# Optimization experiments

Hardware: AMD Instinct MI355X
Metric: run time of the kernel (lower is better)

## Reference

```python
import jax, jax.numpy as jnp
import numpy as np

M, N, T = 4, 48, 512
D_IN = M + N                 # GRU-net input dim (m+n)
H1 = D_IN * 10 * 8           # 4160
HID = M * M + N * N          # 2320 GRU hidden
H2 = M * N * 4               # 768
D_OUT = M * N                # 192


def setup_inputs() -> dict:
    key = jax.random.key(0)
    ks = jax.random.split(key, 12)
    s = lambda i, shape, sc=0.02: (jax.random.normal(ks[i], shape, jnp.float32) * sc)
    return {
        "A": jnp.eye(M, dtype=jnp.float32) + s(0, (M, M), 0.05),
        "C": s(1, (N, M + 1), 0.1),
        "x0": jax.random.normal(ks[2], (M,), jnp.float32),
        "h0": jax.random.normal(ks[3], (HID,), jnp.float32),  # randn init hidden (zero_hidden_state=False)
        "y_seq": jax.random.normal(ks[4], (N, T), jnp.float32),
        "W1": s(5, (H1, D_IN)), "b1": jnp.zeros((H1,), jnp.float32),
        "W_ih": s(6, (3 * HID, H1)), "W_hh": s(7, (3 * HID, HID)),
        "b_ih": jnp.zeros((3 * HID,), jnp.float32), "b_hh": jnp.zeros((3 * HID,), jnp.float32),
        "W2": s(8, (H2, HID)), "b2": jnp.zeros((H2,), jnp.float32),
        "W3": s(9, (D_OUT, H2)), "b3": jnp.zeros((D_OUT,), jnp.float32),
    }


def _l2norm(v):
    # torch F.normalize(p=2, eps=1e-12): v / max(||v||, eps)
    return v / jnp.maximum(jnp.linalg.norm(v), 1e-12)


def _gru_cell(x, h, W_ih, W_hh, b_ih, b_hh):
    gi = W_ih @ x + b_ih
    gh = W_hh @ h + b_hh
    i_r, i_z, i_n = jnp.split(gi, 3)
    h_r, h_z, h_n = jnp.split(gh, 3)
    r = jax.nn.sigmoid(i_r + h_r)
    z = jax.nn.sigmoid(i_z + h_z)
    n = jnp.tanh(i_n + r * h_n)
    return (1.0 - z) * n + z * h


def reference(A, C, x0, h0, y_seq, W1, b1, W_ih, W_hh, b_ih, b_hh, W2, b2, W3, b3):
    one = jnp.ones((1,), jnp.float32)

    def step(carry, y):
        x_prior, x_post, h = carry
        # step_prior (linear case)
        x_prev_prior = x_prior
        x_prior = A @ x_post
        m1y = C @ jnp.concatenate([x_prior, one])  # [N]
        # step_KGain_est: KGainNet_in = [norm(dy), norm(dx)]
        knet_in = jnp.concatenate([_l2norm(y - m1y), _l2norm(x_post - x_prev_prior)])
        l1 = jax.nn.relu(W1 @ knet_in + b1)
        h = _gru_cell(l1, h, W_ih, W_hh, b_ih, b_hh)
        l2 = jax.nn.relu(W2 @ h + b2)
        kg = ((W3 @ l2 + b3) / 10000.0).reshape(M, N)
        # KNet_step posterior update
        x_post = x_prior + kg @ (y - m1y)
        return (x_prior, x_post, h), x_post

    _, xs = jax.lax.scan(step, (x0, x0, h0), y_seq.T)  # scan over T
    return xs.T  # [M, T], matches forward_sequence output
```

## Files before the change

kernel.cpp:

```cpp
#include <hip/hip_runtime.h>
#include <stdint.h>
#include <stddef.h>

typedef float v2f __attribute__((ext_vector_type(2)));

#define HID   2320
#define G3    6960
#define KIH   4160
#define KHH   2320
#define NBLK  232
#define NL2B  192
#define NTHR  512
#define UPB   10
#define TSEQ  512
#define KRES  1600
#define INVWS (1.0f/128.0f)
#define SPINCAP (1u<<17)

#define WS_WIH8 0L
#define WS_W1E  28953600L
#define WS_HBP  29219840L
#define WS_SLT  29279232L
#define WS_END  29308928L

struct Offs {
  int l1s, hs, wih, whh, w2s, w3s, cs, as_, b3s, bih, bhh, b2s, gis, ghs,
      ts, inn, kn, dxs, xpri, xpo, b4, nrm, l2r, slp;
  int total;
};

__host__ __device__ inline Offs mkoffs(int res) {
  Offs o; int p = 0;
#define ALLOC(name, bytes) { p = (p + 15) & ~15; o.name = p; p += (bytes); }
  ALLOC(l1s, KIH*4) ALLOC(hs, HID*4)
  ALLOC(wih, res ? 30*KRES : 16) ALLOC(whh, res ? 30*KHH : 16)
  ALLOC(w2s, res ? 4*HID : 16)
  ALLOC(w3s, 16*48*4) ALLOC(cs, 240*4) ALLOC(as_, 64) ALLOC(b3s, 192*4)
  ALLOC(bih, 120) ALLOC(bhh, 120) ALLOC(b2s, 16)
  ALLOC(gis, 120) ALLOC(ghs, 120)
  ALLOC(ts, 64) ALLOC(inn, 192) ALLOC(kn, 256)
  ALLOC(dxs, 16) ALLOC(xpri, 16) ALLOC(xpo, 16) ALLOC(b4, 16) ALLOC(nrm, 16)
  ALLOC(l2r, 16) ALLOC(slp, 64)
#undef ALLOC
  o.total = (p + 63) & ~63;
  return o;
}

struct Params {
  const float *A, *C, *x0, *h0, *y, *W1, *b1, *Wih, *Whh, *bih, *bhh, *W2, *b2, *W3, *b3;
  const uint8_t *wih8, *w1e;
  uint64_t *hbp, *slt;
  float *out;
  int resident;
};

__device__ __forceinline__ uint8_t f2fp8(float v) {
  v = fminf(fmaxf(v * 128.f, -448.f), 448.f);
  int pk = __builtin_amdgcn_cvt_pk_fp8_f32(v, v, 0, false);
  return (uint8_t)(pk & 0xff);
}

__device__ __forceinline__ void pub64(uint64_t* a, uint32_t tag, float v) {
  uint64_t w = ((uint64_t)tag << 32) | (uint64_t)__float_as_uint(v);
  __hip_atomic_store(a, w, __ATOMIC_RELAXED, __HIP_MEMORY_SCOPE_AGENT);
}

template<int N>
__device__ __forceinline__ void poll_pkt(const uint64_t* base, uint32_t want,
                                         float* out, bool& dead) {
  uint64_t v[N];
  uint32_t spins = 0;
  for (;;) {
    bool ok = true;
#pragma unroll
    for (int k = 0; k < N; ++k)
      v[k] = __hip_atomic_load(base + k, __ATOMIC_RELAXED, __HIP_MEMORY_SCOPE_AGENT);
#pragma unroll
    for (int k = 0; k < N; ++k) ok &= ((uint32_t)(v[k] >> 32) == want);
    if (ok || dead) break;
    ++spins;
    if (spins > 8) __builtin_amdgcn_s_sleep(2);
    if (spins > SPINCAP) dead = true;
  }
#pragma unroll
  for (int k = 0; k < N; ++k) out[k] = __uint_as_float((uint32_t)v[k]);
}

__device__ __forceinline__ void dot8_lds(
    const float* __restrict__ acts, const uint8_t* __restrict__ w, int stride,
    int K, const int* lrows, int nr, int lane, float acc[4])
{
  int kb = 0;
  for (; kb + 256 <= K; kb += 256) {
    const float4 a = ((const float4*)(acts + kb))[lane];
#pragma unroll
    for (int j = 0; j < 4; ++j) if (j < nr) {
      uint32_t wb = *(const uint32_t*)(w + (size_t)lrows[j]*stride + kb + (lane<<2));
      v2f lo = __builtin_amdgcn_cvt_pk_f32_fp8((int)wb, false);
      v2f hi = __builtin_amdgcn_cvt_pk_f32_fp8((int)wb, true);
      acc[j] = fmaf(lo.x, a.x, acc[j]); acc[j] = fmaf(lo.y, a.y, acc[j]);
      acc[j] = fmaf(hi.x, a.z, acc[j]); acc[j] = fmaf(hi.y, a.w, acc[j]);
    }
  }
  int rem = K - kb;
  if ((lane << 2) < rem) {
    const float4 a = ((const float4*)(acts + kb))[lane];
#pragma unroll
    for (int j = 0; j < 4; ++j) if (j < nr) {
      uint32_t wb = *(const uint32_t*)(w + (size_t)lrows[j]*stride + kb + (lane<<2));
      v2f lo = __builtin_amdgcn_cvt_pk_f32_fp8((int)wb, false);
      v2f hi = __builtin_amdgcn_cvt_pk_f32_fp8((int)wb, true);
      acc[j] = fmaf(lo.x, a.x, acc[j]); acc[j] = fmaf(lo.y, a.y, acc[j]);
      acc[j] = fmaf(hi.x, a.z, acc[j]); acc[j] = fmaf(hi.y, a.w, acc[j]);
    }
  }
}

__device__ __forceinline__ void dot8_glb(
    const float* __restrict__ acts, const uint8_t* __restrict__ gw, int gstride,
    int K0, int K, const int* grows, int nr, int lane, float acc[4])
{
  int kb = K0;
  for (; kb + 512 <= K; kb += 512) {
    const float4 a0 = ((const float4*)(acts + kb))[lane*2];
    const float4 a1 = ((const float4*)(acts + kb))[lane*2 + 1];
#pragma unroll
    for (int j = 0; j < 4; ++j) if (j < nr) {
      uint2 wb = *(const uint2*)(gw + (size_t)grows[j]*gstride + kb + (lane<<3));
      v2f l0 = __builtin_amdgcn_cvt_pk_f32_fp8((int)wb.x, false);
      v2f h0 = __builtin_amdgcn_cvt_pk_f32_fp8((int)wb.x, true);
      v2f l1 = __builtin_amdgcn_cvt_pk_f32_fp8((int)wb.y, false);
      v2f h1 = __builtin_amdgcn_cvt_pk_f32_fp8((int)wb.y, true);
      acc[j] = fmaf(l0.x, a0.x, acc[j]); acc[j] = fmaf(l0.y, a0.y, acc[j]);
      acc[j] = fmaf(h0.x, a0.z, acc[j]); acc[j] = fmaf(h0.y, a0.w, acc[j]);
      acc[j] = fmaf(l1.x, a1.x, acc[j]); acc[j] = fmaf(l1.y, a1.y, acc[j]);
      acc[j] = fmaf(h1.x, a1.z, acc[j]); acc[j] = fmaf(h1.y, a1.w, acc[j]);
    }
  }
  for (int e = kb + lane; e < K; e += 64) {
    float a = acts[e];
#pragma unroll
    for (int j = 0; j < 4; ++j) if (j < nr) {
      v2f lo = __builtin_amdgcn_cvt_pk_f32_fp8(
          (int)(uint32_t)gw[(size_t)grows[j]*gstride + e], false);
      acc[j] = fmaf(lo.x, a, acc[j]);
    }
  }
}

__device__ __forceinline__ void dotf_glb(
    const float* __restrict__ acts, const float* __restrict__ gw, int gstride,
    int K, const int* grows, int nr, int lane, float acc[4])
{
  for (int k = lane; k < K; k += 64) {
    float a = acts[k];
#pragma unroll
    for (int j = 0; j < 4; ++j) if (j < nr)
      acc[j] = fmaf(gw[(size_t)grows[j]*gstride + k], a, acc[j]);
  }
}

extern "C" __global__ void __launch_bounds__(NTHR, 2) knet_main(Params p)
{
  extern __shared__ char smem[];
  const Offs o = mkoffs(p.resident);
  float*   L1S  = (float*)(smem + o.l1s);
  float*   HS   = (float*)(smem + o.hs);
  uint8_t* WIHR = (uint8_t*)(smem + o.wih);
  uint8_t* WHHR = (uint8_t*)(smem + o.whh);
  uint8_t* W2S  = (uint8_t*)(smem + o.w2s);
  float*   W3S  = (float*)(smem + o.w3s);
  float*   CS   = (float*)(smem + o.cs);
  float*   AS   = (float*)(smem + o.as_);
  float*   B3S  = (float*)(smem + o.b3s);
  float*   BIH  = (float*)(smem + o.bih);
  float*   BHH  = (float*)(smem + o.bhh);
  float*   B2S  = (float*)(smem + o.b2s);
  float*   GIS  = (float*)(smem + o.gis);
  float*   GHS  = (float*)(smem + o.ghs);
  float*   TS   = (float*)(smem + o.ts);
  float*   INNS = (float*)(smem + o.inn);
  float*   KN   = (float*)(smem + o.kn);
  float*   DXS  = (float*)(smem + o.dxs);
  float*   XPRI = (float*)(smem + o.xpri);
  float*   XPO  = (float*)(smem + o.xpo);
  float*   B4   = (float*)(smem + o.b4);
  float*   NRM  = (float*)(smem + o.nrm);
  float*   L2R  = (float*)(smem + o.l2r);
  float*   SLP  = (float*)(smem + o.slp);

  const int tid  = (int)threadIdx.x;
  const int bid  = (int)blockIdx.x;
  const int lane = tid & 63;
  const int wv   = tid >> 6;
  const int rows2 = (bid < NL2B) ? 4 : 0;
  const int r2s   = bid * 4;
  bool dead = false;

  int lrows[4] = {0,0,0,0}, grows[4] = {0,0,0,0};
  int nr = 0;
#pragma unroll
  for (int j = 0; j < 4; ++j) {
    int row = wv + 8*j;
    if (row < 30) { int u = row/3, g = row - 3*u;
      lrows[nr] = row; grows[nr] = g*HID + bid*UPB + u; ++nr; }
  }

  for (int i = tid; i < rows2*192; i += NTHR) { int rl = i/192, rem = i - rl*192;
    W3S[i] = p.W3[(size_t)rem*768 + (r2s + rl)]; }
  for (int i = tid; i < 240; i += NTHR) CS[i] = p.C[i];
  if (tid < 16) AS[tid] = p.A[tid];
  for (int i = tid; i < 192; i += NTHR) B3S[i] = p.b3[i];
  if (tid < rows2) B2S[tid] = p.b2[r2s + tid];
  if (tid < 30) {
    int u = tid/3, g = tid - 3*u, ug = bid*UPB + u;
    BIH[tid] = p.bih[g*HID + ug];
    BHH[tid] = p.bhh[g*HID + ug];
  }
  for (int i = tid; i < HID; i += NTHR) HS[i] = p.h0[i];
  if (p.resident) {
    const int kd = KRES >> 2;
    uint32_t* W32 = (uint32_t*)WIHR;
    for (int i = tid; i < 30*kd; i += NTHR) {
      int row = i / kd, c = i - row*kd;
      int u = row/3, g = row - 3*u, gr = g*HID + bid*UPB + u;
      W32[i] = ((const uint32_t*)p.wih8)[(size_t)gr*(KIH/4) + c];
    }
    for (int i = tid; i < 30*KHH; i += NTHR) {
      int row = i / KHH, k = i - row*KHH;
      int u = row/3, g = row - 3*u, gr = g*HID + bid*UPB + u;
      WHHR[i] = f2fp8(p.Whh[(size_t)gr*KHH + k]);
    }
    for (int i = tid; i < rows2*HID; i += NTHR) {
      int rl = i / HID, k = i - rl*HID;
      W2S[i] = f2fp8(p.W2[(size_t)(r2s+rl)*HID + k]);
    }
  }
  uint2 pf[4][5];
#pragma unroll
  for (int j = 0; j < 4; ++j)
#pragma unroll
    for (int i = 0; i < 5; ++i) pf[j][i] = make_uint2(0u, 0u);
#pragma unroll
  for (int j = 0; j < 4; ++j) if (j < nr)
#pragma unroll
    for (int i = 0; i < 5; ++i)
      pf[j][i] = *(const uint2*)(p.wih8 + (size_t)grows[j]*KIH + KRES + i*512 + (lane<<3));
  __syncthreads();

  auto small_chain = [&](int ycol) {
    if (tid < 48) {
      float s = CS[tid*5 + 4];
#pragma unroll
      for (int k = 0; k < 4; ++k) s += CS[tid*5 + k] * XPRI[k];
      INNS[tid] = p.y[(size_t)tid*TSEQ + ycol] - s;
    }
    __syncthreads();
    if (wv == 0) {
      float q = (lane < 48) ? INNS[lane]*INNS[lane] : 0.f;
#pragma unroll
      for (int m = 32; m >= 1; m >>= 1) q += __shfl_xor(q, m, 64);
      if (lane == 0) NRM[0] = fmaxf(sqrtf(q), 1e-12f);
    } else if (wv == 1) {
      float q = (lane < 4) ? DXS[lane]*DXS[lane] : 0.f;
#pragma unroll
      for (int m = 32; m >= 1; m >>= 1) q += __shfl_xor(q, m, 64);
      if (lane == 0) NRM[1] = fmaxf(sqrtf(q), 1e-12f);
    }
    __syncthreads();
    if (tid < 48) KN[tid] = INNS[tid] / NRM[0];
    else if (tid < 52) KN[tid] = DXS[tid-48] / NRM[1];
    else if (tid == 52) KN[tid] = 1.0f;
    else if (tid < 64) KN[tid] = 0.0f;
    else if (tid < 68) {
      int i = tid - 64; float s = 0;
      for (int j = 0; j < 48; ++j) s += B3S[i*48 + j] * INNS[j];
      B4[i] = s;
    }
    if (tid >= 128 && tid < 128 + rows2*4) {
      int idx = tid - 128, rl = idx >> 2, i = idx & 3;
      float s = 0;
      for (int j = 0; j < 48; ++j) s += W3S[rl*192 + i*48 + j] * INNS[j];
      TS[i*4 + rl] = s;
    }
    __syncthreads();
    {
      float4 kn[16];
#pragma unroll
      for (int c = 0; c < 16; ++c) kn[c] = ((const float4*)KN)[c];
      for (int r = tid; r < KIH; r += NTHR) {
        const uint4* wp = (const uint4*)(p.w1e + (size_t)r*64);
        float acc = 0.f;
#pragma unroll
        for (int q = 0; q < 4; ++q) {
          uint4 w = wp[q];
          v2f l0 = __builtin_amdgcn_cvt_pk_f32_fp8((int)w.x, false);
          v2f h0 = __builtin_amdgcn_cvt_pk_f32_fp8((int)w.x, true);
          v2f l1 = __builtin_amdgcn_cvt_pk_f32_fp8((int)w.y, false);
          v2f h1 = __builtin_amdgcn_cvt_pk_f32_fp8((int)w.y, true);
          v2f l2 = __builtin_amdgcn_cvt_pk_f32_fp8((int)w.z, false);
          v2f h2 = __builtin_amdgcn_cvt_pk_f32_fp8((int)w.z, true);
          v2f l3 = __builtin_amdgcn_cvt_pk_f32_fp8((int)w.w, false);
          v2f h3 = __builtin_amdgcn_cvt_pk_f32_fp8((int)w.w, true);
          float4 a0 = kn[q*4+0], a1 = kn[q*4+1], a2 = kn[q*4+2], a3 = kn[q*4+3];
          acc = fmaf(l0.x,a0.x,acc); acc = fmaf(l0.y,a0.y,acc);
          acc = fmaf(h0.x,a0.z,acc); acc = fmaf(h0.y,a0.w,acc);
          acc = fmaf(l1.x,a1.x,acc); acc = fmaf(l1.y,a1.y,acc);
          acc = fmaf(h1.x,a1.z,acc); acc = fmaf(h1.y,a1.w,acc);
          acc = fmaf(l2.x,a2.x,acc); acc = fmaf(l2.y,a2.y,acc);
          acc = fmaf(h2.x,a2.z,acc); acc = fmaf(h2.y,a2.w,acc);
          acc = fmaf(l3.x,a3.x,acc); acc = fmaf(l3.y,a3.y,acc);
          acc = fmaf(h3.x,a3.z,acc); acc = fmaf(h3.y,a3.w,acc);
        }
        L1S[r] = fmaxf(acc * INVWS, 0.f);
      }
    }
    __syncthreads();
  };

  auto ghh = [&]() {
    float acc[4] = {0,0,0,0};
    if (p.resident) dot8_lds(HS, WHHR, KHH, KHH, lrows, nr, lane, acc);
    else            dotf_glb(HS, p.Whh, KHH, KHH, grows, nr, lane, acc);
#pragma unroll
    for (int m = 32; m >= 1; m >>= 1)
#pragma unroll
      for (int j = 0; j < 4; ++j) acc[j] += __shfl_xor(acc[j], m, 64);
    if (lane == 0)
#pragma unroll
      for (int j = 0; j < 4; ++j) if (j < nr) GHS[lrows[j]] = acc[j];
  };

  if (tid < 4) { XPO[tid] = p.x0[tid]; DXS[tid] = 0.f; }
  __syncthreads();
  if (tid < 4) {
    float s = 0;
#pragma unroll
    for (int j = 0; j < 4; ++j) s += AS[tid*4 + j] * XPO[j];
    XPRI[tid] = s;
  }
  __syncthreads();
  small_chain(0);
  ghh();
  __syncthreads();

  for (int t = 0; t < TSEQ; ++t) {
    const int par = t & 1;
    const uint32_t want = (uint32_t)(t + 1);

    {
      float acc[4] = {0,0,0,0};
      if (p.resident) dot8_lds(L1S, WIHR, KRES, KRES, lrows, nr, lane, acc);
      else            dot8_glb(L1S, p.wih8, KIH, 0, KRES, grows, nr, lane, acc);
#pragma unroll
      for (int i = 0; i < 5; ++i) {
        const float4 a0 = ((const float4*)(L1S + KRES + i*512))[lane*2];
        const float4 a1 = ((const float4*)(L1S + KRES + i*512))[lane*2 + 1];
#pragma unroll
        for (int j = 0; j < 4; ++j) if (j < nr) {
          uint2 w = pf[j][i];
          v2f l0 = __builtin_amdgcn_cvt_pk_f32_fp8((int)w.x, false);
          v2f h0 = __builtin_amdgcn_cvt_pk_f32_fp8((int)w.x, true);
          v2f l1v = __builtin_amdgcn_cvt_pk_f32_fp8((int)w.y, false);
          v2f h1 = __builtin_amdgcn_cvt_pk_f32_fp8((int)w.y, true);
          acc[j] = fmaf(l0.x, a0.x, acc[j]); acc[j] = fmaf(l0.y, a0.y, acc[j]);
          acc[j] = fmaf(h0.x, a0.z, acc[j]); acc[j] = fmaf(h0.y, a0.w, acc[j]);
          acc[j] = fmaf(l1v.x, a1.x, acc[j]); acc[j] = fmaf(l1v.y, a1.y, acc[j]);
          acc[j] = fmaf(h1.x, a1.z, acc[j]); acc[j] = fmaf(h1.y, a1.w, acc[j]);
        }
      }
#pragma unroll
      for (int m = 32; m >= 1; m >>= 1)
#pragma unroll
        for (int j = 0; j < 4; ++j) acc[j] += __shfl_xor(acc[j], m, 64);
      if (lane == 0)
#pragma unroll
        for (int j = 0; j < 4; ++j) if (j < nr) GIS[lrows[j]] = acc[j];
    }
    __syncthreads();

    if (tid < UPB) {
      int ug = bid*UPB + tid, r0 = tid*3;
      float gi0 = GIS[r0+0]*INVWS + BIH[r0+0], gh0 = GHS[r0+0]*INVWS + BHH[r0+0];
      float gi1 = GIS[r0+1]*INVWS + BIH[r0+1], gh1 = GHS[r0+1]*INVWS + BHH[r0+1];
      float gi2 = GIS[r0+2]*INVWS + BIH[r0+2], gh2 = GHS[r0+2]*INVWS + BHH[r0+2];
      float rg = 1.f/(1.f + expf(-(gi0+gh0)));
      float zg = 1.f/(1.f + expf(-(gi1+gh1)));
      float ng = tanhf(gi2 + rg*gh2);
      float hnew = (1.f - zg)*ng + zg*HS[ug];
      pub64(p.hbp + (((size_t)par*NBLK + bid) << 4) + tid, want, hnew);
    }
    __syncthreads();

    if (wv < 4) {
      int idx = (wv << 6) | lane;
      if (idx < NBLK) {
        float v[10];
        poll_pkt<10>(p.hbp + (((size_t)par*NBLK + idx) << 4), want, v, dead);
#pragma unroll
        for (int k = 0; k < 10; ++k) HS[idx*10 + k] = v[k];
      }
    }
    __syncthreads();

    if (rows2 && wv >= 4) {
      const int rl = wv - 4;
      float a2 = 0.f;
      if (p.resident) {
        int kb = 0;
        for (; kb + 256 <= HID; kb += 256) {
          const float4 a = ((const float4*)(HS + kb))[lane];
          uint32_t wb = *(const uint32_t*)(W2S + rl*HID + kb + (lane<<2));
          v2f lo = __builtin_amdgcn_cvt_pk_f32_fp8((int)wb, false);
          v2f hi = __builtin_amdgcn_cvt_pk_f32_fp8((int)wb, true);
          a2 = fmaf(lo.x, a.x, a2); a2 = fmaf(lo.y, a.y, a2);
          a2 = fmaf(hi.x, a.z, a2); a2 = fmaf(hi.y, a.w, a2);
        }
        if ((lane << 2) < HID - kb) {
          const float4 a = ((const float4*)(HS + kb))[lane];
          uint32_t wb = *(const uint32_t*)(W2S + rl*HID + kb + (lane<<2));
          v2f lo = __builtin_amdgcn_cvt_pk_f32_fp8((int)wb, false);
          v2f hi = __builtin_amdgcn_cvt_pk_f32_fp8((int)wb, true);
          a2 = fmaf(lo.x, a.x, a2); a2 = fmaf(lo.y, a.y, a2);
          a2 = fmaf(hi.x, a.z, a2); a2 = fmaf(hi.y, a.w, a2);
        }
        a2 *= INVWS;
      } else {
        for (int k = lane; k < HID; k += 64)
          a2 = fmaf(p.W2[(size_t)(r2s+rl)*HID + k], HS[k], a2);
      }
#pragma unroll
      for (int m = 32; m >= 1; m >>= 1) a2 += __shfl_xor(a2, m, 64);
      if (lane == 0) L2R[rl] = fmaxf(a2 + B2S[rl], 0.f);
    }
    __syncthreads();
    if (rows2 && tid < 4) {
      float cp = L2R[0]*TS[tid*4+0] + L2R[1]*TS[tid*4+1]
               + L2R[2]*TS[tid*4+2] + L2R[3]*TS[tid*4+3];
      pub64(p.slt + (((size_t)par*NBLK + bid) << 3) + tid, want, cp);
    }

    ghh();

    if (wv < 3) {
      int idx = (wv << 6) | lane;
      float v[4];
      poll_pkt<4>(p.slt + (((size_t)par*NBLK + idx) << 3), want, v, dead);
      float s0 = v[0], s1 = v[1], s2 = v[2], s3 = v[3];
#pragma unroll
      for (int m = 32; m >= 1; m >>= 1) {
        s0 += __shfl_xor(s0, m, 64); s1 += __shfl_xor(s1, m, 64);
        s2 += __shfl_xor(s2, m, 64); s3 += __shfl_xor(s3, m, 64);
      }
      if (lane == 0) {
        SLP[wv*4+0] = s0; SLP[wv*4+1] = s1; SLP[wv*4+2] = s2; SLP[wv*4+3] = s3;
      }
    }
    __syncthreads();

    if (tid < 4) {
      float c = SLP[tid] + SLP[4 + tid] + SLP[8 + tid];
      float xp = XPRI[tid] + (c + B4[tid]) * 1e-4f;
      XPO[tid] = xp;
      if (bid == 0) p.out[(size_t)tid*TSEQ + t] = xp;
    }
    __syncthreads();
    if (t + 1 < TSEQ) {
      if (tid < 4) {
        float xo = XPO[tid];
        DXS[tid] = xo - XPRI[tid];
        float s = 0;
#pragma unroll
        for (int j = 0; j < 4; ++j) s += AS[tid*4 + j] * XPO[j];
        XPRI[tid] = s;
      }
      __syncthreads();
      small_chain(t + 1);
    }
  }
}

extern "C" __global__ void knet_cvt_fp8(const float* __restrict__ src,
                                        uint8_t* __restrict__ dst, long n4) {
  long stride = (long)gridDim.x * blockDim.x;
  for (long i = (long)blockIdx.x*blockDim.x + threadIdx.x; i < n4; i += stride) {
    float4 v = ((const float4*)src)[i];
    float a0 = fminf(fmaxf(v.x * 128.f, -448.f), 448.f);
    float a1 = fminf(fmaxf(v.y * 128.f, -448.f), 448.f);
    float a2 = fminf(fmaxf(v.z * 128.f, -448.f), 448.f);
    float a3 = fminf(fmaxf(v.w * 128.f, -448.f), 448.f);
    int pk = __builtin_amdgcn_cvt_pk_fp8_f32(a0, a1, 0, false);
    pk = __builtin_amdgcn_cvt_pk_fp8_f32(a2, a3, pk, true);
    ((uint32_t*)dst)[i] = (uint32_t)pk;
  }
}

extern "C" __global__ void knet_build_w1e(const float* __restrict__ W1,
                                          const float* __restrict__ b1,
                                          uint8_t* __restrict__ dst) {
  int r = blockIdx.x * blockDim.x + threadIdx.x;
  if (r >= KIH) return;
  float v[64];
#pragma unroll 13
  for (int q = 0; q < 13; ++q) {
    float4 w = ((const float4*)(W1 + (size_t)r*52))[q];
    v[q*4+0] = w.x; v[q*4+1] = w.y; v[q*4+2] = w.z; v[q*4+3] = w.w;
  }
  v[52] = b1[r];
  for (int i = 53; i < 64; ++i) v[i] = 0.f;
  uint32_t out[16];
#pragma unroll 16
  for (int d = 0; d < 16; ++d) {
    float a0 = fminf(fmaxf(v[d*4+0] * 128.f, -448.f), 448.f);
    float a1 = fminf(fmaxf(v[d*4+1] * 128.f, -448.f), 448.f);
    float a2 = fminf(fmaxf(v[d*4+2] * 128.f, -448.f), 448.f);
    float a3 = fminf(fmaxf(v[d*4+3] * 128.f, -448.f), 448.f);
    int pk = __builtin_amdgcn_cvt_pk_fp8_f32(a0, a1, 0, false);
    pk = __builtin_amdgcn_cvt_pk_fp8_f32(a2, a3, pk, true);
    out[d] = (uint32_t)pk;
  }
  uint4* dp = (uint4*)(dst + (size_t)r*64);
#pragma unroll 4
  for (int q = 0; q < 4; ++q)
    dp[q] = make_uint4(out[q*4+0], out[q*4+1], out[q*4+2], out[q*4+3]);
}

extern "C" void kernel_launch(void* const* d_in, const int* in_sizes, int n_in,
                              void* d_out, int out_size, void* d_ws, size_t ws_size,
                              hipStream_t stream)
{
  if (ws_size < (size_t)WS_END) return;
  uint8_t* ws = (uint8_t*)d_ws;

  knet_cvt_fp8<<<2048, 256, 0, stream>>>((const float*)d_in[7], ws + WS_WIH8,
                                         (long)G3*KIH/4);
  knet_build_w1e<<<(KIH + 255)/256, 256, 0, stream>>>(
      (const float*)d_in[5], (const float*)d_in[6], ws + WS_W1E);

  int resident = 1;
  Offs o = mkoffs(resident);
  hipError_t e = hipFuncSetAttribute((const void*)knet_main,
                                     hipFuncAttributeMaxDynamicSharedMemorySize,
                                     o.total);
  if (e != hipSuccess) {
    resident = 0; o = mkoffs(resident);
    (void)hipFuncSetAttribute((const void*)knet_main,
                              hipFuncAttributeMaxDynamicSharedMemorySize, o.total);
  }

  Params p;
  p.A   = (const float*)d_in[0];  p.C   = (const float*)d_in[1];
  p.x0  = (const float*)d_in[2];  p.h0  = (const float*)d_in[3];
  p.y   = (const float*)d_in[4];
  p.W1  = (const float*)d_in[5];  p.b1  = (const float*)d_in[6];
  p.Wih = (const float*)d_in[7];  p.Whh = (const float*)d_in[8];
  p.bih = (const float*)d_in[9];  p.bhh = (const float*)d_in[10];
  p.W2  = (const float*)d_in[11]; p.b2  = (const float*)d_in[12];
  p.W3  = (const float*)d_in[13]; p.b3  = (const float*)d_in[14];
  p.wih8 = ws + WS_WIH8;
  p.w1e  = ws + WS_W1E;
  p.hbp  = (uint64_t*)(ws + WS_HBP);
  p.slt  = (uint64_t*)(ws + WS_SLT);
  p.out  = (float*)d_out;
  p.resident = resident;

  knet_main<<<NBLK, NTHR, (size_t)o.total, stream>>>(p);
}
```

Before: 8.289 ms.

## Keep W1 rows in registers, poll single flag first, drop GRU barrier

Each thread now preloads the first four 512-row chunks of the fp8 W1 matrix into registers once, so the per-step layer-1 matvec reads those rows from registers instead of global memory. The GRU hidden element owned by each thread is kept in a register (myh), which removes the read of HS and allows the barrier between publishing h and polling peers to be dropped. Polling now spins on the first packet word alone before checking the rest, which cuts the number of atomic loads per spin iteration. The cost is higher register pressure, about 64 extra VGPRs for the W1 cache, which may lower occupancy or cause spills.

```diff
diff --git a/kernel.cpp b/kernel.cpp
--- a/kernel.cpp
+++ b/kernel.cpp
@@ -14,6 +14,7 @@
 #define UPB   10
 #define TSEQ  512
 #define KRES  1600
+#define HQ    4
 #define INVWS (1.0f/128.0f)
 #define SPINCAP (1u<<17)
 
@@ -68,22 +69,55 @@
 template<int N>
 __device__ __forceinline__ void poll_pkt(const uint64_t* base, uint32_t want,
                                          float* out, bool& dead) {
-  uint64_t v[N];
+  uint64_t v0;
   uint32_t spins = 0;
   for (;;) {
-    bool ok = true;
-#pragma unroll
-    for (int k = 0; k < N; ++k)
-      v[k] = __hip_atomic_load(base + k, __ATOMIC_RELAXED, __HIP_MEMORY_SCOPE_AGENT);
-#pragma unroll
-    for (int k = 0; k < N; ++k) ok &= ((uint32_t)(v[k] >> 32) == want);
-    if (ok || dead) break;
+    v0 = __hip_atomic_load(base, __ATOMIC_RELAXED, __HIP_MEMORY_SCOPE_AGENT);
+    if ((uint32_t)(v0 >> 32) == want || dead) break;
     ++spins;
-    if (spins > 8) __builtin_amdgcn_s_sleep(2);
+    if (spins > 32) __builtin_amdgcn_s_sleep(2);
     if (spins > SPINCAP) dead = true;
   }
-#pragma unroll
-  for (int k = 0; k < N; ++k) out[k] = __uint_as_float((uint32_t)v[k]);
+  out[0] = __uint_as_float((uint32_t)v0);
+  if (N > 1) {
+    uint64_t v[N];
+    uint32_t s2 = 0;
+    for (;;) {
+      bool ok = true;
+#pragma unroll
+      for (int k = 1; k < N; ++k)
+        v[k] = __hip_atomic_load(base + k, __ATOMIC_RELAXED, __HIP_MEMORY_SCOPE_AGENT);
+#pragma unroll
+      for (int k = 1; k < N; ++k) ok &= ((uint32_t)(v[k] >> 32) == want);
+      if (ok || dead) break;
+      ++s2;
+      if (s2 > 8) __builtin_amdgcn_s_sleep(2);
+      if (s2 > SPINCAP) dead = true;
+    }
+#pragma unroll
+    for (int k = 1; k < N; ++k) out[k] = __uint_as_float((uint32_t)v[k]);
+  }
+}
+
+__device__ __forceinline__ float fma16(uint4 w, float4 a0, float4 a1,
+                                       float4 a2, float4 a3, float acc) {
+  v2f l0 = __builtin_amdgcn_cvt_pk_f32_fp8((int)w.x, false);
+  v2f h0 = __builtin_amdgcn_cvt_pk_f32_fp8((int)w.x, true);
+  v2f l1 = __builtin_amdgcn_cvt_pk_f32_fp8((int)w.y, false);
+  v2f h1 = __builtin_amdgcn_cvt_pk_f32_fp8((int)w.y, true);
+  v2f l2 = __builtin_amdgcn_cvt_pk_f32_fp8((int)w.z, false);
+  v2f h2 = __builtin_amdgcn_cvt_pk_f32_fp8((int)w.z, true);
+  v2f l3 = __builtin_amdgcn_cvt_pk_f32_fp8((int)w.w, false);
+  v2f h3 = __builtin_amdgcn_cvt_pk_f32_fp8((int)w.w, true);
+  acc = fmaf(l0.x,a0.x,acc); acc = fmaf(l0.y,a0.y,acc);
+  acc = fmaf(h0.x,a0.z,acc); acc = fmaf(h0.y,a0.w,acc);
+  acc = fmaf(l1.x,a1.x,acc); acc = fmaf(l1.y,a1.y,acc);
+  acc = fmaf(h1.x,a1.z,acc); acc = fmaf(h1.y,a1.w,acc);
+  acc = fmaf(l2.x,a2.x,acc); acc = fmaf(l2.y,a2.y,acc);
+  acc = fmaf(h2.x,a2.z,acc); acc = fmaf(h2.y,a2.w,acc);
+  acc = fmaf(l3.x,a3.x,acc); acc = fmaf(l3.y,a3.y,acc);
+  acc = fmaf(h3.x,a3.z,acc); acc = fmaf(h3.y,a3.w,acc);
+  return acc;
 }
 
 __device__ __forceinline__ void dot8_lds(
@@ -218,6 +252,7 @@
     BHH[tid] = p.bhh[g*HID + ug];
   }
   for (int i = tid; i < HID; i += NTHR) HS[i] = p.h0[i];
+  float myh = (tid < UPB) ? p.h0[(size_t)bid*UPB + tid] : 0.f;
   if (p.resident) {
     const int kd = KRES >> 2;
     uint32_t* W32 = (uint32_t*)WIHR;
@@ -246,6 +281,13 @@
 #pragma unroll
     for (int i = 0; i < 5; ++i)
       pf[j][i] = *(const uint2*)(p.wih8 + (size_t)grows[j]*KIH + KRES + i*512 + (lane<<3));
+  uint4 w1h[HQ][4];
+#pragma unroll
+  for (int h = 0; h < HQ; ++h) {
+    const uint4* wp = (const uint4*)(p.w1e + (size_t)(tid + h*NTHR)*64);
+#pragma unroll
+    for (int q = 0; q < 4; ++q) w1h[h][q] = wp[q];
+  }
   __syncthreads();
 
   auto small_chain = [&](int ycol) {
@@ -288,29 +330,21 @@
       float4 kn[16];
 #pragma unroll
       for (int c = 0; c < 16; ++c) kn[c] = ((const float4*)KN)[c];
-      for (int r = tid; r < KIH; r += NTHR) {
+#pragma unroll
+      for (int h = 0; h < HQ; ++h) {
+        float acc = 0.f;
+#pragma unroll
+        for (int q = 0; q < 4; ++q)
+          acc = fma16(w1h[h][q], kn[q*4+0], kn[q*4+1], kn[q*4+2], kn[q*4+3], acc);
+        L1S[tid + h*NTHR] = fmaxf(acc * INVWS, 0.f);
+      }
+      for (int r = tid + HQ*NTHR; r < KIH; r += NTHR) {
         const uint4* wp = (const uint4*)(p.w1e + (size_t)r*64);
         float acc = 0.f;
 #pragma unroll
         for (int q = 0; q < 4; ++q) {
           uint4 w = wp[q];
-          v2f l0 = __builtin_amdgcn_cvt_pk_f32_fp8((int)w.x, false);
-          v2f h0 = __builtin_amdgcn_cvt_pk_f32_fp8((int)w.x, true);
-          v2f l1 = __builtin_amdgcn_cvt_pk_f32_fp8((int)w.y, false);
-          v2f h1 = __builtin_amdgcn_cvt_pk_f32_fp8((int)w.y, true);
-          v2f l2 = __builtin_amdgcn_cvt_pk_f32_fp8((int)w.z, false);
-          v2f h2 = __builtin_amdgcn_cvt_pk_f32_fp8((int)w.z, true);
-          v2f l3 = __builtin_amdgcn_cvt_pk_f32_fp8((int)w.w, false);
-          v2f h3 = __builtin_amdgcn_cvt_pk_f32_fp8((int)w.w, true);
-          float4 a0 = kn[q*4+0], a1 = kn[q*4+1], a2 = kn[q*4+2], a3 = kn[q*4+3];
-          acc = fmaf(l0.x,a0.x,acc); acc = fmaf(l0.y,a0.y,acc);
-          acc = fmaf(h0.x,a0.z,acc); acc = fmaf(h0.y,a0.w,acc);
-          acc = fmaf(l1.x,a1.x,acc); acc = fmaf(l1.y,a1.y,acc);
-          acc = fmaf(h1.x,a1.z,acc); acc = fmaf(h1.y,a1.w,acc);
-          acc = fmaf(l2.x,a2.x,acc); acc = fmaf(l2.y,a2.y,acc);
-          acc = fmaf(h2.x,a2.z,acc); acc = fmaf(h2.y,a2.w,acc);
-          acc = fmaf(l3.x,a3.x,acc); acc = fmaf(l3.y,a3.y,acc);
-          acc = fmaf(h3.x,a3.z,acc); acc = fmaf(h3.y,a3.w,acc);
+          acc = fma16(w, kn[q*4+0], kn[q*4+1], kn[q*4+2], kn[q*4+3], acc);
         }
         L1S[r] = fmaxf(acc * INVWS, 0.f);
       }
@@ -380,17 +414,17 @@
     __syncthreads();
 
     if (tid < UPB) {
-      int ug = bid*UPB + tid, r0 = tid*3;
+      int r0 = tid*3;
       float gi0 = GIS[r0+0]*INVWS + BIH[r0+0], gh0 = GHS[r0+0]*INVWS + BHH[r0+0];
       float gi1 = GIS[r0+1]*INVWS + BIH[r0+1], gh1 = GHS[r0+1]*INVWS + BHH[r0+1];
       float gi2 = GIS[r0+2]*INVWS + BIH[r0+2], gh2 = GHS[r0+2]*INVWS + BHH[r0+2];
       float rg = 1.f/(1.f + expf(-(gi0+gh0)));
       float zg = 1.f/(1.f + expf(-(gi1+gh1)));
       float ng = tanhf(gi2 + rg*gh2);
-      float hnew = (1.f - zg)*ng + zg*HS[ug];
+      float hnew = (1.f - zg)*ng + zg*myh;
+      myh = hnew;
       pub64(p.hbp + (((size_t)par*NBLK + bid) << 4) + tid, want, hnew);
     }
-    __syncthreads();
 
     if (wv < 4) {
       int idx = (wv << 6) | lane;
```

Measured after the change: 28.31 ms. 3.41x slower.

## Precompute next-step W1 innovation product early and overlap it with GRU stages

Applied to the files above, without the earlier changes.

The innovation for step t+1 is split algebraically into a part that depends only on the prior state, y_{t+1} - C·A·x_prior, and a correction that is linear in dx. The W1 product for that first part is computed in chunks on idle waves during the hidden-state gather, layer-2 and ghh phases, so the serial per-step layer-1 matvec shrinks to a cheap finish pass. The finish pass applies the dx correction through precomputed W1·C·A columns stored as fp16 in spare w1e slots, then normalises, adds the bias and applies ReLU. The own-unit hidden value is kept in a register, which lets one barrier be dropped. The cost is added numerical approximation from the fp16/fp8 correction terms and more complex scheduling across waves.

```diff
diff --git a/kernel.cpp b/kernel.cpp
--- a/kernel.cpp
+++ b/kernel.cpp
@@ -1,4 +1,5 @@
 #include <hip/hip_runtime.h>
+#include <hip/hip_fp16.h>
 #include <stdint.h>
 #include <stddef.h>
 
@@ -14,6 +15,8 @@
 #define UPB   10
 #define TSEQ  512
 #define KRES  1600
+#define CH0   2080
+#define CH1   2336
 #define INVWS (1.0f/128.0f)
 #define SPINCAP (1u<<17)
 
@@ -25,7 +28,7 @@
 
 struct Offs {
   int l1s, hs, wih, whh, w2s, w3s, cs, as_, b3s, bih, bhh, b2s, gis, ghs,
-      ts, inn, kn, dxs, xpri, xpo, b4, nrm, l2r, slp;
+      ts, inn, inn0, xq, cma, dxs, xpri, xpo, b4, nrm, l2r, slp;
   int total;
 };
 
@@ -38,7 +41,7 @@
   ALLOC(w3s, 16*48*4) ALLOC(cs, 240*4) ALLOC(as_, 64) ALLOC(b3s, 192*4)
   ALLOC(bih, 120) ALLOC(bhh, 120) ALLOC(b2s, 16)
   ALLOC(gis, 120) ALLOC(ghs, 120)
-  ALLOC(ts, 64) ALLOC(inn, 192) ALLOC(kn, 256)
+  ALLOC(ts, 64) ALLOC(inn, 192) ALLOC(inn0, 192) ALLOC(xq, 16) ALLOC(cma, 768)
   ALLOC(dxs, 16) ALLOC(xpri, 16) ALLOC(xpo, 16) ALLOC(b4, 16) ALLOC(nrm, 16)
   ALLOC(l2r, 16) ALLOC(slp, 64)
 #undef ALLOC
@@ -84,6 +87,27 @@
   }
 #pragma unroll
   for (int k = 0; k < N; ++k) out[k] = __uint_as_float((uint32_t)v[k]);
+}
+
+__device__ __forceinline__ float fma16(uint4 w, float4 a0, float4 a1,
+                                       float4 a2, float4 a3, float acc) {
+  v2f l0 = __builtin_amdgcn_cvt_pk_f32_fp8((int)w.x, false);
+  v2f h0 = __builtin_amdgcn_cvt_pk_f32_fp8((int)w.x, true);
+  v2f l1 = __builtin_amdgcn_cvt_pk_f32_fp8((int)w.y, false);
+  v2f h1 = __builtin_amdgcn_cvt_pk_f32_fp8((int)w.y, true);
+  v2f l2 = __builtin_amdgcn_cvt_pk_f32_fp8((int)w.z, false);
+  v2f h2 = __builtin_amdgcn_cvt_pk_f32_fp8((int)w.z, true);
+  v2f l3 = __builtin_amdgcn_cvt_pk_f32_fp8((int)w.w, false);
+  v2f h3 = __builtin_amdgcn_cvt_pk_f32_fp8((int)w.w, true);
+  acc = fmaf(l0.x,a0.x,acc); acc = fmaf(l0.y,a0.y,acc);
+  acc = fmaf(h0.x,a0.z,acc); acc = fmaf(h0.y,a0.w,acc);
+  acc = fmaf(l1.x,a1.x,acc); acc = fmaf(l1.y,a1.y,acc);
+  acc = fmaf(h1.x,a1.z,acc); acc = fmaf(h1.y,a1.w,acc);
+  acc = fmaf(l2.x,a2.x,acc); acc = fmaf(l2.y,a2.y,acc);
+  acc = fmaf(h2.x,a2.z,acc); acc = fmaf(h2.y,a2.w,acc);
+  acc = fmaf(l3.x,a3.x,acc); acc = fmaf(l3.y,a3.y,acc);
+  acc = fmaf(h3.x,a3.z,acc); acc = fmaf(h3.y,a3.w,acc);
+  return acc;
 }
 
 __device__ __forceinline__ void dot8_lds(
@@ -180,7 +204,9 @@
   float*   GHS  = (float*)(smem + o.ghs);
   float*   TS   = (float*)(smem + o.ts);
   float*   INNS = (float*)(smem + o.inn);
-  float*   KN   = (float*)(smem + o.kn);
+  float*   INN0 = (float*)(smem + o.inn0);
+  float*   XQ   = (float*)(smem + o.xq);
+  float*   CMA  = (float*)(smem + o.cma);
   float*   DXS  = (float*)(smem + o.dxs);
   float*   XPRI = (float*)(smem + o.xpri);
   float*   XPO  = (float*)(smem + o.xpo);
@@ -218,6 +244,7 @@
     BHH[tid] = p.bhh[g*HID + ug];
   }
   for (int i = tid; i < HID; i += NTHR) HS[i] = p.h0[i];
+  float myh = (tid < UPB) ? p.h0[(size_t)bid*UPB + tid] : 0.f;
   if (p.resident) {
     const int kd = KRES >> 2;
     uint32_t* W32 = (uint32_t*)WIHR;
@@ -248,74 +275,43 @@
       pf[j][i] = *(const uint2*)(p.wih8 + (size_t)grows[j]*KIH + KRES + i*512 + (lane<<3));
   __syncthreads();
 
-  auto small_chain = [&](int ycol) {
-    if (tid < 48) {
-      float s = CS[tid*5 + 4];
-#pragma unroll
-      for (int k = 0; k < 4; ++k) s += CS[tid*5 + k] * XPRI[k];
-      INNS[tid] = p.y[(size_t)tid*TSEQ + ycol] - s;
-    }
-    __syncthreads();
-    if (wv == 0) {
-      float q = (lane < 48) ? INNS[lane]*INNS[lane] : 0.f;
-#pragma unroll
-      for (int m = 32; m >= 1; m >>= 1) q += __shfl_xor(q, m, 64);
-      if (lane == 0) NRM[0] = fmaxf(sqrtf(q), 1e-12f);
-    } else if (wv == 1) {
-      float q = (lane < 4) ? DXS[lane]*DXS[lane] : 0.f;
-#pragma unroll
-      for (int m = 32; m >= 1; m >>= 1) q += __shfl_xor(q, m, 64);
-      if (lane == 0) NRM[1] = fmaxf(sqrtf(q), 1e-12f);
-    }
-    __syncthreads();
-    if (tid < 48) KN[tid] = INNS[tid] / NRM[0];
-    else if (tid < 52) KN[tid] = DXS[tid-48] / NRM[1];
-    else if (tid == 52) KN[tid] = 1.0f;
-    else if (tid < 64) KN[tid] = 0.0f;
-    else if (tid < 68) {
-      int i = tid - 64; float s = 0;
-      for (int j = 0; j < 48; ++j) s += B3S[i*48 + j] * INNS[j];
-      B4[i] = s;
-    }
-    if (tid >= 128 && tid < 128 + rows2*4) {
-      int idx = tid - 128, rl = idx >> 2, i = idx & 3;
-      float s = 0;
-      for (int j = 0; j < 48; ++j) s += W3S[rl*192 + i*48 + j] * INNS[j];
-      TS[i*4 + rl] = s;
-    }
-    __syncthreads();
-    {
-      float4 kn[16];
-#pragma unroll
-      for (int c = 0; c < 16; ++c) kn[c] = ((const float4*)KN)[c];
-      for (int r = tid; r < KIH; r += NTHR) {
-        const uint4* wp = (const uint4*)(p.w1e + (size_t)r*64);
-        float acc = 0.f;
-#pragma unroll
-        for (int q = 0; q < 4; ++q) {
-          uint4 w = wp[q];
-          v2f l0 = __builtin_amdgcn_cvt_pk_f32_fp8((int)w.x, false);
-          v2f h0 = __builtin_amdgcn_cvt_pk_f32_fp8((int)w.x, true);
-          v2f l1 = __builtin_amdgcn_cvt_pk_f32_fp8((int)w.y, false);
-          v2f h1 = __builtin_amdgcn_cvt_pk_f32_fp8((int)w.y, true);
-          v2f l2 = __builtin_amdgcn_cvt_pk_f32_fp8((int)w.z, false);
-          v2f h2 = __builtin_amdgcn_cvt_pk_f32_fp8((int)w.z, true);
-          v2f l3 = __builtin_amdgcn_cvt_pk_f32_fp8((int)w.w, false);
-          v2f h3 = __builtin_amdgcn_cvt_pk_f32_fp8((int)w.w, true);
-          float4 a0 = kn[q*4+0], a1 = kn[q*4+1], a2 = kn[q*4+2], a3 = kn[q*4+3];
-          acc = fmaf(l0.x,a0.x,acc); acc = fmaf(l0.y,a0.y,acc);
-          acc = fmaf(h0.x,a0.z,acc); acc = fmaf(h0.y,a0.w,acc);
-          acc = fmaf(l1.x,a1.x,acc); acc = fmaf(l1.y,a1.y,acc);
-          acc = fmaf(h1.x,a1.z,acc); acc = fmaf(h1.y,a1.w,acc);
-          acc = fmaf(l2.x,a2.x,acc); acc = fmaf(l2.y,a2.y,acc);
-          acc = fmaf(h2.x,a2.z,acc); acc = fmaf(h2.y,a2.w,acc);
-          acc = fmaf(l3.x,a3.x,acc); acc = fmaf(l3.y,a3.y,acc);
-          acc = fmaf(h3.x,a3.z,acc); acc = fmaf(h3.y,a3.w,acc);
-        }
-        L1S[r] = fmaxf(acc * INVWS, 0.f);
-      }
-    }
-    __syncthreads();
+  if (tid < 192) {
+    int j = tid >> 2, k = tid & 3;
+    CMA[tid] = CS[j*5+0]*AS[0*4+k] + CS[j*5+1]*AS[1*4+k]
+             + CS[j*5+2]*AS[2*4+k] + CS[j*5+3]*AS[3*4+k];
+  }
+
+  auto l1a_chunk = [&](int lo, int hi, int tbase, int tcnt) {
+    float4 in0[12];
+#pragma unroll
+    for (int c = 0; c < 12; ++c) in0[c] = ((const float4*)INN0)[c];
+    for (int r = lo + (tid - tbase); r < hi; r += tcnt) {
+      const uint4* wp = (const uint4*)(p.w1e + (size_t)r*64);
+      uint4 w0 = wp[0], w1 = wp[1], w2 = wp[2];
+      float acc = 0.f;
+      acc = fma16(w0, in0[0], in0[1], in0[2],  in0[3],  acc);
+      acc = fma16(w1, in0[4], in0[5], in0[6],  in0[7],  acc);
+      acc = fma16(w2, in0[8], in0[9], in0[10], in0[11], acc);
+      L1S[r] = acc;
+    }
+  };
+
+  auto l1_finish = [&]() {
+    float d0 = DXS[0], d1 = DXS[1], d2 = DXS[2], d3 = DXS[3];
+    float invn0 = 1.f / NRM[0], invn1 = 1.f / NRM[1];
+    float n0 = d0*invn1, n1 = d1*invn1, n2 = d2*invn1, n3 = d3*invn1;
+    for (int r = tid; r < KIH; r += NTHR) {
+      uint4 w = *(const uint4*)(p.w1e + (size_t)r*64 + 48);
+      v2f dq0 = __builtin_amdgcn_cvt_pk_f32_fp8((int)w.x, false);
+      v2f dq1 = __builtin_amdgcn_cvt_pk_f32_fp8((int)w.x, true);
+      v2f bq  = __builtin_amdgcn_cvt_pk_f32_fp8((int)w.y, false);
+      float2 c01 = __half22float2(*(const __half2*)&w.z);
+      float2 c23 = __half22float2(*(const __half2*)&w.w);
+      float corr = c01.x*d0 + c01.y*d1 + c23.x*d2 + c23.y*d3;
+      float acc = (L1S[r] - corr) * invn0
+                + dq0.x*n0 + dq0.y*n1 + dq1.x*n2 + dq1.y*n3 + bq.x;
+      L1S[r] = fmaxf(acc * INVWS, 0.f);
+    }
   };
 
   auto ghh = [&]() {
@@ -340,7 +336,51 @@
     XPRI[tid] = s;
   }
   __syncthreads();
-  small_chain(0);
+  if (tid < 48) {
+    float s = CS[tid*5 + 4];
+#pragma unroll
+    for (int k = 0; k < 4; ++k) s += CS[tid*5 + k] * XPRI[k];
+    float i0 = p.y[(size_t)tid*TSEQ + 0] - s;
+    INN0[tid] = i0; INNS[tid] = i0;
+  } else if (tid >= 64 && tid < 68) {
+    int k = tid - 64; float s = 0;
+#pragma unroll
+    for (int j = 0; j < 4; ++j) s += AS[k*4 + j] * XPRI[j];
+    XQ[k] = s;
+  }
+  __syncthreads();
+  if (wv == 0) {
+    float q = (lane < 48) ? INNS[lane]*INNS[lane] : 0.f;
+#pragma unroll
+    for (int m = 32; m >= 1; m >>= 1) q += __shfl_xor(q, m, 64);
+    if (lane == 0) NRM[0] = fmaxf(sqrtf(q), 1e-12f);
+  } else if (wv == 1) {
+    float q = (lane < 4) ? DXS[lane]*DXS[lane] : 0.f;
+#pragma unroll
+    for (int m = 32; m >= 1; m >>= 1) q += __shfl_xor(q, m, 64);
+    if (lane == 0) NRM[1] = fmaxf(sqrtf(q), 1e-12f);
+  }
+  if (tid >= 128 && tid < 132) {
+    int i = tid - 128; float s = 0;
+    for (int j = 0; j < 48; ++j) s += B3S[i*48 + j] * INNS[j];
+    B4[i] = s;
+  }
+  if (rows2 && tid >= 192 && tid < 208) {
+    int idx = tid - 192, rl = idx >> 2, i = idx & 3;
+    float s = 0;
+    for (int j = 0; j < 48; ++j) s += W3S[rl*192 + i*48 + j] * INNS[j];
+    TS[i*4 + rl] = s;
+  }
+  __syncthreads();
+  l1a_chunk(0, KIH, 0, NTHR);
+  l1_finish();
+  __syncthreads();
+  if (tid < 48) {
+    float s = CS[tid*5 + 4];
+#pragma unroll
+    for (int k = 0; k < 4; ++k) s += CS[tid*5 + k] * XQ[k];
+    INN0[tid] = p.y[(size_t)tid*TSEQ + 1] - s;
+  }
   ghh();
   __syncthreads();
 
@@ -380,17 +420,17 @@
     __syncthreads();
 
     if (tid < UPB) {
-      int ug = bid*UPB + tid, r0 = tid*3;
+      int r0 = tid*3;
       float gi0 = GIS[r0+0]*INVWS + BIH[r0+0], gh0 = GHS[r0+0]*INVWS + BHH[r0+0];
       float gi1 = GIS[r0+1]*INVWS + BIH[r0+1], gh1 = GHS[r0+1]*INVWS + BHH[r0+1];
       float gi2 = GIS[r0+2]*INVWS + BIH[r0+2], gh2 = GHS[r0+2]*INVWS + BHH[r0+2];
       float rg = 1.f/(1.f + expf(-(gi0+gh0)));
       float zg = 1.f/(1.f + expf(-(gi1+gh1)));
       float ng = tanhf(gi2 + rg*gh2);
-      float hnew = (1.f - zg)*ng + zg*HS[ug];
+      float hnew = (1.f - zg)*ng + zg*myh;
+      myh = hnew;
       pub64(p.hbp + (((size_t)par*NBLK + bid) << 4) + tid, want, hnew);
     }
-    __syncthreads();
 
     if (wv < 4) {
       int idx = (wv << 6) | lane;
@@ -400,6 +440,8 @@
 #pragma unroll
         for (int k = 0; k < 10; ++k) HS[idx*10 + k] = v[k];
       }
+    } else if (t + 1 < TSEQ) {
+      l1a_chunk(0, CH0, 256, 256);
     }
     __syncthreads();
 
@@ -432,6 +474,8 @@
 #pragma unroll
       for (int m = 32; m >= 1; m >>= 1) a2 += __shfl_xor(a2, m, 64);
       if (lane == 0) L2R[rl] = fmaxf(a2 + B2S[rl], 0.f);
+    } else if (wv < 4 && t + 1 < TSEQ) {
+      l1a_chunk(CH0, CH1, 0, 256);
     }
     __syncthreads();
     if (rows2 && tid < 4) {
@@ -441,6 +485,7 @@
     }
 
     ghh();
+    if (t + 1 < TSEQ) l1a_chunk(CH1, KIH, 0, NTHR);
 
     if (wv < 3) {
       int idx = (wv << 6) | lane;
@@ -465,6 +510,7 @@
       if (bid == 0) p.out[(size_t)tid*TSEQ + t] = xp;
     }
     __syncthreads();
+
     if (t + 1 < TSEQ) {
       if (tid < 4) {
         float xo = XPO[tid];
@@ -475,7 +521,48 @@
         XPRI[tid] = s;
       }
       __syncthreads();
-      small_chain(t + 1);
+      if (tid < 48) {
+        float dv = CMA[tid*4+0]*DXS[0] + CMA[tid*4+1]*DXS[1]
+                 + CMA[tid*4+2]*DXS[2] + CMA[tid*4+3]*DXS[3];
+        INNS[tid] = INN0[tid] - dv;
+      } else if (tid >= 64 && tid < 68) {
+        int k = tid - 64; float s = 0;
+#pragma unroll
+        for (int j = 0; j < 4; ++j) s += AS[k*4 + j] * XPRI[j];
+        XQ[k] = s;
+      }
+      __syncthreads();
+      if (wv == 0) {
+        float q = (lane < 48) ? INNS[lane]*INNS[lane] : 0.f;
+#pragma unroll
+        for (int m = 32; m >= 1; m >>= 1) q += __shfl_xor(q, m, 64);
+        if (lane == 0) NRM[0] = fmaxf(sqrtf(q), 1e-12f);
+      } else if (wv == 1) {
+        float q = (lane < 4) ? DXS[lane]*DXS[lane] : 0.f;
+#pragma unroll
+        for (int m = 32; m >= 1; m >>= 1) q += __shfl_xor(q, m, 64);
+        if (lane == 0) NRM[1] = fmaxf(sqrtf(q), 1e-12f);
+      }
+      if (tid >= 128 && tid < 132) {
+        int i = tid - 128; float s = 0;
+        for (int j = 0; j < 48; ++j) s += B3S[i*48 + j] * INNS[j];
+        B4[i] = s;
+      }
+      if (rows2 && tid >= 192 && tid < 208) {
+        int idx = tid - 192, rl = idx >> 2, i = idx & 3;
+        float s = 0;
+        for (int j = 0; j < 48; ++j) s += W3S[rl*192 + i*48 + j] * INNS[j];
+        TS[i*4 + rl] = s;
+      }
+      __syncthreads();
+      if (tid < 48 && t + 2 < TSEQ) {
+        float s = CS[tid*5 + 4];
+#pragma unroll
+        for (int k = 0; k < 4; ++k) s += CS[tid*5 + k] * XQ[k];
+        INN0[tid] = p.y[(size_t)tid*TSEQ + (t+2)] - s;
+      }
+      l1_finish();
+      __syncthreads();
     }
   }
 }
@@ -497,6 +584,8 @@
 
 extern "C" __global__ void knet_build_w1e(const float* __restrict__ W1,
                                           const float* __restrict__ b1,
+                                          const float* __restrict__ Cm,
+                                          const float* __restrict__ Am,
                                           uint8_t* __restrict__ dst) {
   int r = blockIdx.x * blockDim.x + threadIdx.x;
   if (r >= KIH) return;
@@ -519,6 +608,27 @@
     pk = __builtin_amdgcn_cvt_pk_fp8_f32(a2, a3, pk, true);
     out[d] = (uint32_t)pk;
   }
+  float w4[4];
+#pragma unroll
+  for (int k = 0; k < 4; ++k) {
+    float a0 = Am[0*4+k], a1 = Am[1*4+k], a2 = Am[2*4+k], a3 = Am[3*4+k];
+    float acc = 0.f;
+    for (int q = 0; q < 12; ++q) {
+      v2f lo = __builtin_amdgcn_cvt_pk_f32_fp8((int)out[q], false);
+      v2f hi = __builtin_amdgcn_cvt_pk_f32_fp8((int)out[q], true);
+      int j = q * 4;
+      float c0 = Cm[(j+0)*5+0]*a0 + Cm[(j+0)*5+1]*a1 + Cm[(j+0)*5+2]*a2 + Cm[(j+0)*5+3]*a3;
+      float c1 = Cm[(j+1)*5+0]*a0 + Cm[(j+1)*5+1]*a1 + Cm[(j+1)*5+2]*a2 + Cm[(j+1)*5+3]*a3;
+      float c2 = Cm[(j+2)*5+0]*a0 + Cm[(j+2)*5+1]*a1 + Cm[(j+2)*5+2]*a2 + Cm[(j+2)*5+3]*a3;
+      float c3 = Cm[(j+3)*5+0]*a0 + Cm[(j+3)*5+1]*a1 + Cm[(j+3)*5+2]*a2 + Cm[(j+3)*5+3]*a3;
+      acc += lo.x*c0 + lo.y*c1 + hi.x*c2 + hi.y*c3;
+    }
+    w4[k] = acc;
+  }
+  __half2 h01 = __floats2half2_rn(w4[0], w4[1]);
+  __half2 h23 = __floats2half2_rn(w4[2], w4[3]);
+  out[14] = *(const uint32_t*)&h01;
+  out[15] = *(const uint32_t*)&h23;
   uint4* dp = (uint4*)(dst + (size_t)r*64);
 #pragma unroll 4
   for (int q = 0; q < 4; ++q)
@@ -535,7 +645,8 @@
   knet_cvt_fp8<<<2048, 256, 0, stream>>>((const float*)d_in[7], ws + WS_WIH8,
                                          (long)G3*KIH/4);
   knet_build_w1e<<<(KIH + 255)/256, 256, 0, stream>>>(
-      (const float*)d_in[5], (const float*)d_in[6], ws + WS_W1E);
+      (const float*)d_in[5], (const float*)d_in[6],
+      (const float*)d_in[1], (const float*)d_in[0], ws + WS_W1E);
 
   int resident = 1;
   Offs o = mkoffs(resident);
```

Result: slower. 10.64 ms (+28.4%).
